# Kernel optimization log

Hardware: AMD Instinct MI355X
Metric: run time of the kernel (lower is better)

The kernel has to match this reference:

```python
import jax, jax.numpy as jnp
import numpy as np

NUM_OBS_OS = 8
NUM_OBS_TS = 6
HIDDEN = 128
NUM_ACTIONS = 9
B = 32768
N_TS = 32


def setup_inputs() -> dict:
    key = jax.random.key(0)
    ks = jax.random.split(key, 16)
    s_OS = jax.random.normal(ks[0], (B, NUM_OBS_OS), dtype=jnp.float32)
    s_TS = jax.random.normal(ks[1], (B, N_TS, NUM_OBS_TS), dtype=jnp.float32)
    # variable number of valid target ships per row (0..N_TS); trailing slots -> NaN
    lengths = jax.random.randint(ks[2], (B,), 0, N_TS + 1)
    pad = jnp.arange(N_TS)[None, :] >= lengths[:, None]          # [B, N_TS]
    s_TS = jnp.where(pad[:, :, None], jnp.nan, s_TS)
    s = jnp.concatenate([s_OS, s_TS.reshape(B, N_TS * NUM_OBS_TS)], axis=1)

    def lin(k, out_d, in_d):
        bound = 1.0 / np.sqrt(in_d)
        kw, kb = jax.random.split(k)
        W = jax.random.uniform(kw, (out_d, in_d), jnp.float32, -bound, bound)
        b = jax.random.uniform(kb, (out_d,), jnp.float32, -bound, bound)
        return W, b

    W_os, b_os = lin(ks[3], HIDDEN, NUM_OBS_OS)
    bound = 1.0 / np.sqrt(HIDDEN)
    W_ih = jax.random.uniform(ks[4], (4 * HIDDEN, NUM_OBS_TS), jnp.float32, -bound, bound)
    W_hh = jax.random.uniform(ks[5], (4 * HIDDEN, HIDDEN), jnp.float32, -bound, bound)
    b_ih = jax.random.uniform(ks[6], (4 * HIDDEN,), jnp.float32, -bound, bound)
    b_hh = jax.random.uniform(ks[7], (4 * HIDDEN,), jnp.float32, -bound, bound)
    W_ts, b_ts = lin(ks[8], HIDDEN, HIDDEN)
    W_c1, b_c1 = lin(ks[9], HIDDEN, 2 * HIDDEN)
    W_c2, b_c2 = lin(ks[10], NUM_ACTIONS, HIDDEN)
    return {"s": s, "W_os": W_os, "b_os": b_os, "W_ih": W_ih, "W_hh": W_hh,
            "b_ih": b_ih, "b_hh": b_hh, "W_ts": W_ts, "b_ts": b_ts,
            "W_c1": W_c1, "b_c1": b_c1, "W_c2": W_c2, "b_c2": b_c2}


def _lstm(x, W_ih, W_hh, b_ih, b_hh):
    """Single-layer batch-first LSTM; x: [B, T, I] -> outputs [B, T, H]."""
    Bc, T, _ = x.shape
    H = W_hh.shape[1]
    # precompute input projections for all steps: [T, B, 4H]
    xg = jnp.einsum('bti,gi->tbg', x, W_ih) + (b_ih + b_hh)

    def step(carry, xt):
        h, c = carry
        gates = xt + h @ W_hh.T                      # [B, 4H]
        i, f, g, o = jnp.split(gates, 4, axis=-1)    # torch order: i, f, g, o
        i = jax.nn.sigmoid(i)
        f = jax.nn.sigmoid(f)
        g = jnp.tanh(g)
        o = jax.nn.sigmoid(o)
        c = f * c + i * g
        h = o * jnp.tanh(c)
        return (h, c), h

    h0 = jnp.zeros((Bc, H), x.dtype)
    c0 = jnp.zeros((Bc, H), x.dtype)
    _, hs = jax.lax.scan(step, (h0, c0), xg)         # hs: [T, B, H]
    return jnp.transpose(hs, (1, 0, 2))


def reference(s, W_os, b_os, W_ih, W_hh, b_ih, b_hh, W_ts, b_ts, W_c1, b_c1, W_c2, b_c2):
    Bc = s.shape[0]
    s_OS = s[:, :NUM_OBS_OS]
    s_TS = s[:, NUM_OBS_OS:].reshape(Bc, -1, NUM_OBS_TS)          # [B, N_TS, 6]
    valid = jnp.logical_not(jnp.isnan(s_TS[:, :, 0]))             # [B, N_TS]
    n_obs = jnp.sum(valid, axis=1)                                # [B]
    h_idx = jnp.maximum(n_obs, 1) - 1                             # last valid step
    s_TS = jnp.where(jnp.isnan(s_TS), 0.0, s_TS)

    x_OS = jax.nn.relu(s_OS @ W_os.T + b_os)                      # [B, 128]

    out = _lstm(s_TS, W_ih, W_hh, b_ih, b_hh)                     # [B, N_TS, 128]
    x_TS = jnp.take_along_axis(out, h_idx[:, None, None], axis=1)[:, 0]  # [B, 128]
    x_TS = jnp.where((n_obs == 0)[:, None], 0.0, x_TS)
    x_TS = jax.nn.relu(x_TS @ W_ts.T + b_ts)

    x = jnp.concatenate([x_OS, x_TS], axis=1)                     # [B, 256]
    x = jax.nn.relu(x @ W_c1.T + b_c1)
    return x @ W_c2.T + b_c2                                      # [B, num_actions]
```

## Files before the change

kernel.cpp:

```cpp
#include <hip/hip_runtime.h>

#ifndef __has_builtin
#define __has_builtin(x) 0
#endif

#define NOBS_OS 8
#define NOBS_TS 6
#define HID 128
#define NACT 9
#define BTOT 32768
#define NTS 32
#define ROWS 16
#define NTILES 2048
#define QUADS 512
#define BLOCK 512
#define PREB 128

#define LEN_OFF 0
#define PERM_OFF BTOT
#define HIST_OFF (2 * BTOT)

typedef __attribute__((ext_vector_type(8))) short short8;
typedef __attribute__((ext_vector_type(4))) float f32x4;

__device__ inline unsigned short f2bf(float x) {
  unsigned int u = __float_as_uint(x);
  u += 0x7FFFu + ((u >> 16) & 1u);
  return (unsigned short)(u >> 16);
}

__device__ inline unsigned pkbf(float a, float b) {
#if __has_builtin(__builtin_amdgcn_cvt_pk_bf16_f32)
  auto v = __builtin_amdgcn_cvt_pk_bf16_f32(a, b);
  unsigned u;
  __builtin_memcpy(&u, &v, sizeof(u));
  return u;
#else
  return ((unsigned)f2bf(b) << 16) | (unsigned)f2bf(a);
#endif
}

__device__ inline float fexp2(float x) {
#if __has_builtin(__builtin_amdgcn_exp2f)
  return __builtin_amdgcn_exp2f(x);
#else
  return exp2f(x);
#endif
}
__device__ inline float frcp_(float x) {
#if __has_builtin(__builtin_amdgcn_rcpf)
  return __builtin_amdgcn_rcpf(x);
#else
  return 1.0f / x;
#endif
}

__device__ inline short8 pack8(f32x4 a, f32x4 b) {
  union { unsigned u[4]; short8 s; } r;
  r.u[0] = pkbf(a[0], a[1]); r.u[1] = pkbf(a[2], a[3]);
  r.u[2] = pkbf(b[0], b[1]); r.u[3] = pkbf(b[2], b[3]);
  return r.s;
}

__device__ inline short8 pack8s(const float* p, float s) {
  union { unsigned u[4]; short8 r; } r;
#pragma unroll
  for (int i = 0; i < 4; ++i) r.u[i] = pkbf(p[2 * i] * s, p[2 * i + 1] * s);
  return r.r;
}

__global__ void count_kernel(const float* __restrict__ s, int* __restrict__ ws) {
  __shared__ int lh[NTS + 1];
  const int tid = threadIdx.x;
  if (tid <= NTS) lh[tid] = 0;
  __syncthreads();
  const int row = blockIdx.x * 256 + tid;
  const float* p = s + (size_t)row * 200 + NOBS_OS;
  int lo = 0, hi = NTS;
  while (lo < hi) {
    const int mid = (lo + hi) >> 1;
    const float v = p[mid * NOBS_TS];
    if (v == v) lo = mid + 1; else hi = mid;
  }
  ws[LEN_OFF + row] = lo;
  atomicAdd(&lh[lo], 1);
  __syncthreads();
  if (tid <= NTS) ws[HIST_OFF + blockIdx.x * (NTS + 1) + tid] = lh[tid];
}

__global__ void scatter_kernel(int* __restrict__ ws) {
  __shared__ int tot[NTS + 1], pre[NTS + 1], gb[NTS + 1], lh[NTS + 1];
  const int tid = threadIdx.x;
  if (tid <= NTS) {
    int t = 0, pr = 0;
    for (int k = 0; k < PREB; ++k) {
      const int h = ws[HIST_OFF + k * (NTS + 1) + tid];
      t += h;
      if (k < (int)blockIdx.x) pr += h;
    }
    tot[tid] = t;
    pre[tid] = pr;
    lh[tid] = 0;
  }
  __syncthreads();
  if (tid == 0) {
    int a = 0;
    for (int b = 0; b <= NTS; ++b) { gb[b] = a; a += tot[b]; }
  }
  __syncthreads();
  const int row = blockIdx.x * 256 + tid;
  const int len = ws[LEN_OFF + row];
  const int r = atomicAdd(&lh[len], 1);
  __syncthreads();
  ws[PERM_OFF + gb[len] + pre[len] + r] = row;
}


#define GX(CN, T)                                                            \
  {                                                                          \
    short8 ax = z8;                                                          \
    if (q == 0) ax = *(const short8*)&x_st[CN][c * 264 + (T) * 8];           \
    _Pragma("unroll") for (int a = 0; a < 4; ++a)                            \
        acc[CN][a] = __builtin_amdgcn_mfma_f32_16x16x32_bf16(                \
            ax, Bh[a][4], biasv[a], 0, 0, 0);                                \
  }

#define GH(CN, T)                                                            \
  {                                                                          \
    const unsigned short* hb = hA[CN][((T) + 1) & 1];                        \
    _Pragma("unroll") for (int kt = 0; kt < 4; ++kt) {                       \
      const short8 ah = *(const short8*)&hb[kt * 512 + L * 8];               \
      _Pragma("unroll") for (int a = 0; a < 4; ++a)                          \
          acc[CN][a] = __builtin_amdgcn_mfma_f32_16x16x32_bf16(              \
              ah, Bh[a][kt], acc[CN][a], 0, 0, 0);                           \
    }                                                                        \
  }

#define ACT(CN, T)                                                           \
  {                                                                          \
    unsigned short* hw = &hA[CN][(T) & 1][pbase];                            \
    float hv[4];                                                             \
    _Pragma("unroll") for (int r = 0; r < 4; ++r) {                          \
      const float ei = fexp2(acc[CN][0][r]);                                 \
      const float ef = fexp2(acc[CN][1][r]);                                 \
      const float eg = fexp2(acc[CN][2][r]);                                 \
      const float eo = fexp2(acc[CN][3][r]);                                 \
      const float rig = frcp_((1.0f + ei) * (1.0f + eg));                    \
      const float rf = frcp_(1.0f + ef);                                     \
      const float cv = cc[CN][r] * rf + (1.0f - eg) * rig;                   \
      cc[CN][r] = cv;                                                        \
      const float ec = fexp2(cv * -2.88539008f);                             \
      const float roc = frcp_((1.0f + eo) * (1.0f + ec));                    \
      hv[r] = (1.0f - ec) * roc;                                             \
    }                                                                        \
    const unsigned p01 = pkbf(hv[0], hv[1]);                                 \
    const unsigned p23 = pkbf(hv[2], hv[3]);                                 \
    hw[0] = (unsigned short)p01;                                             \
    hw[8] = (unsigned short)(p01 >> 16);                                     \
    hw[16] = (unsigned short)p23;                                            \
    hw[24] = (unsigned short)(p23 >> 16);                                    \
    _Pragma("unroll") for (int r = 0; r < 4; ++r) {                          \
      if (((tpck[CN] >> (r * 8)) & 255u) == (unsigned)(T))                   \
        xts[CN][r] = hv[r];                                                  \
    }                                                                        \
  }

__global__ __launch_bounds__(BLOCK, 2) void recdqn_kernel(
    const float* __restrict__ s, const float* __restrict__ W_os,
    const float* __restrict__ b_os, const float* __restrict__ W_ih,
    const float* __restrict__ W_hh, const float* __restrict__ b_ih,
    const float* __restrict__ b_hh, const float* __restrict__ W_ts,
    const float* __restrict__ b_ts, const float* __restrict__ W_c1,
    const float* __restrict__ b_c1, const float* __restrict__ W_c2,
    const float* __restrict__ b_c2, const int* __restrict__ ws,
    float* __restrict__ out) {
  __shared__ unsigned short x_st[4][ROWS * 264];
  __shared__ unsigned short hA[4][2][2048];
  __shared__ unsigned short xtsb[4][2048];
  __shared__ unsigned short xcat[4096];
  __shared__ unsigned short x2b[2048];
  __shared__ int n_lds[4][ROWS];
  __shared__ int rid_s[4][ROWS];
  __shared__ int tmax_sh[4];

  const int tid = threadIdx.x;
  const int L = tid & 63;
  const int w = tid >> 6;
  const int c = L & 15;
  const int q = L >> 4;
  const int j = (w << 4) | c;

  const short8 z8 = {0, 0, 0, 0, 0, 0, 0, 0};

  short8 Bh[4][5];
  f32x4 biasv[4];
#pragma unroll
  for (int a = 0; a < 4; ++a) {
    const float sc = (a == 2) ? -2.88539008f : -1.44269504f;
    const int n = (a << 7) + j;
    const float bb = sc * (b_ih[n] + b_hh[n]);
    f32x4 bv = {bb, bb, bb, bb};
    biasv[a] = bv;
#pragma unroll
    for (int kt = 0; kt < 4; ++kt)
      Bh[a][kt] = pack8s(W_hh + n * HID + kt * 32 + q * 8, sc);
    short8 fx = z8;
    if (q == 0) {
      const float* px = W_ih + n * NOBS_TS;
      union { unsigned u[4]; short8 s; } fu;
      fu.u[0] = pkbf(px[0] * sc, px[1] * sc);
      fu.u[1] = pkbf(px[2] * sc, px[3] * sc);
      fu.u[2] = pkbf(px[4] * sc, px[5] * sc);
      fu.u[3] = 0;
      fx = fu.s;
    }
    Bh[a][4] = fx;
  }

  const int pbase = ((j >> 5) << 9) + (((j >> 3) & 3) << 7) + (q << 5) + (j & 7);

  const int p = (QUADS - 1) - blockIdx.x;
  if (tid < 64) {
    const int cn = tid >> 4, rr = tid & 15;
    const int row = ws[PERM_OFF + (4 * p + cn) * ROWS + rr];
    rid_s[cn][rr] = row;
    n_lds[cn][rr] = ws[LEN_OFF + row];
  }
  __syncthreads();

#pragma unroll
  for (int it = 0; it < 4; ++it) {
    const int slot = tid + it * 512;
    const int cn = slot >> 9, rt = slot & 511, r = rt >> 5, tq = rt & 31;
    short8 v = z8;
    if (tq < n_lds[cn][r]) {
      const float2* ps =
          (const float2*)(s + (size_t)rid_s[cn][r] * 200 + NOBS_OS + tq * NOBS_TS);
      const float2 A = ps[0], Bv = ps[1], Cv = ps[2];
      union { unsigned u[4]; short8 s; } vu;
      vu.u[0] = pkbf(A.x, A.y);
      vu.u[1] = pkbf(Bv.x, Bv.y);
      vu.u[2] = pkbf(Cv.x, Cv.y);
      vu.u[3] = 0;
      v = vu.s;
    }
    *(short8*)&x_st[cn][r * 264 + tq * 8] = v;
  }
  if (tid == 0) {
#pragma unroll
    for (int cn = 0; cn < 4; ++cn) {
      int mx = 0;
      for (int r = 0; r < ROWS; ++r) mx = max(mx, n_lds[cn][r]);
      tmax_sh[cn] = mx;
    }
  }
  __syncthreads();

  const int tm0 = tmax_sh[0], tm1 = tmax_sh[1];
  const int tm2 = tmax_sh[2], tm3 = tmax_sh[3];
  unsigned tpck[4];
#pragma unroll
  for (int cn = 0; cn < 4; ++cn) {
    unsigned pk = 0;
#pragma unroll
    for (int b = 0; b < 4; ++b)
      pk |= ((unsigned)((n_lds[cn][q * 4 + b] - 1) & 255)) << (b * 8);
    tpck[cn] = pk;
  }

  float cc[4][4], xts[4][4];
#pragma unroll
  for (int i = 0; i < 4; ++i) {
    cc[0][i] = 0.0f; cc[1][i] = 0.0f; cc[2][i] = 0.0f; cc[3][i] = 0.0f;
    xts[0][i] = 0.0f; xts[1][i] = 0.0f; xts[2][i] = 0.0f; xts[3][i] = 0.0f;
  }

  f32x4 acc[4][4];
  if (tm3 > 0) {
    if (tm0 > 0) GX(0, 0)
    if (tm1 > 0) GX(1, 0)
    if (tm2 > 0) GX(2, 0)
    GX(3, 0)
    if (tm0 > 0) ACT(0, 0)
    if (tm1 > 0) ACT(1, 0)
    if (tm2 > 0) ACT(2, 0)
    ACT(3, 0)
    __syncthreads();
    int t = 1;
    for (; t < tm0; ++t) {
      GX(0, t) GH(0, t)
      GX(1, t) GH(1, t)
      GX(2, t) GH(2, t)
      GX(3, t) GH(3, t)
      ACT(0, t) ACT(1, t) ACT(2, t) ACT(3, t)
      __syncthreads();
    }
    for (; t < tm1; ++t) {
      GX(1, t) GH(1, t)
      GX(2, t) GH(2, t)
      GX(3, t) GH(3, t)
      ACT(1, t) ACT(2, t) ACT(3, t)
      __syncthreads();
    }
    for (; t < tm2; ++t) {
      GX(2, t) GH(2, t)
      GX(3, t) GH(3, t)
      ACT(2, t) ACT(3, t)
      __syncthreads();
    }
    for (; t < tm3; ++t) {
      GX(3, t) GH(3, t)
      ACT(3, t)
      __syncthreads();
    }
  }

#pragma unroll
  for (int cn = 0; cn < 4; ++cn) {
    const unsigned p01 = pkbf(xts[cn][0], xts[cn][1]);
    const unsigned p23 = pkbf(xts[cn][2], xts[cn][3]);
    unsigned short* pw = &xtsb[cn][pbase];
    pw[0] = (unsigned short)p01;
    pw[8] = (unsigned short)(p01 >> 16);
    pw[16] = (unsigned short)p23;
    pw[24] = (unsigned short)(p23 >> 16);
  }
  __syncthreads();

  short8 Fts[4], Fc1[8], Fc2[4], bosf = z8;
#pragma unroll
  for (int kt = 0; kt < 4; ++kt) {
    const f32x4* pp = (const f32x4*)(W_ts + j * HID + kt * 32 + q * 8);
    Fts[kt] = pack8(pp[0], pp[1]);
  }
#pragma unroll
  for (int kt = 0; kt < 8; ++kt) {
    const f32x4* pp = (const f32x4*)(W_c1 + j * 256 + kt * 32 + q * 8);
    Fc1[kt] = pack8(pp[0], pp[1]);
  }
#pragma unroll
  for (int kt = 0; kt < 4; ++kt) Fc2[kt] = z8;
  if (w == 0 && c < NACT) {
#pragma unroll
    for (int kt = 0; kt < 4; ++kt) {
      const f32x4* pp = (const f32x4*)(W_c2 + c * HID + kt * 32 + q * 8);
      Fc2[kt] = pack8(pp[0], pp[1]);
    }
  }
  if (q == 0) {
    const f32x4* pb = (const f32x4*)(W_os + j * NOBS_OS);
    bosf = pack8(pb[0], pb[1]);
  }
  const float bts = b_ts[j], bc1 = b_c1[j], bos = b_os[j];
  const float bc2 = (w == 0 && c < NACT) ? b_c2[c] : 0.0f;

#pragma unroll 1
  for (int cn = 0; cn < 4; ++cn) {
    {
      f32x4 a2 = {bts, bts, bts, bts};
#pragma unroll
      for (int kt = 0; kt < 4; ++kt) {
        const short8 af = *(const short8*)&xtsb[cn][kt * 512 + L * 8];
        a2 = __builtin_amdgcn_mfma_f32_16x16x32_bf16(af, Fts[kt], a2, 0, 0, 0);
      }
      const unsigned p01 = pkbf(fmaxf(a2[0], 0.0f), fmaxf(a2[1], 0.0f));
      const unsigned p23 = pkbf(fmaxf(a2[2], 0.0f), fmaxf(a2[3], 0.0f));
      xcat[2048 + pbase + 0] = (unsigned short)p01;
      xcat[2048 + pbase + 8] = (unsigned short)(p01 >> 16);
      xcat[2048 + pbase + 16] = (unsigned short)p23;
      xcat[2048 + pbase + 24] = (unsigned short)(p23 >> 16);
    }
    {
      short8 aos = z8;
      if (q == 0) {
        const f32x4* pa = (const f32x4*)(s + (size_t)rid_s[cn][c] * 200);
        aos = pack8(pa[0], pa[1]);
      }
      f32x4 a2 = {bos, bos, bos, bos};
      a2 = __builtin_amdgcn_mfma_f32_16x16x32_bf16(aos, bosf, a2, 0, 0, 0);
      const unsigned p01 = pkbf(fmaxf(a2[0], 0.0f), fmaxf(a2[1], 0.0f));
      const unsigned p23 = pkbf(fmaxf(a2[2], 0.0f), fmaxf(a2[3], 0.0f));
      xcat[pbase + 0] = (unsigned short)p01;
      xcat[pbase + 8] = (unsigned short)(p01 >> 16);
      xcat[pbase + 16] = (unsigned short)p23;
      xcat[pbase + 24] = (unsigned short)(p23 >> 16);
    }
    __syncthreads();
    {
      f32x4 a2 = {bc1, bc1, bc1, bc1};
#pragma unroll
      for (int kt = 0; kt < 8; ++kt) {
        const short8 af = *(const short8*)&xcat[kt * 512 + L * 8];
        a2 = __builtin_amdgcn_mfma_f32_16x16x32_bf16(af, Fc1[kt], a2, 0, 0, 0);
      }
      const unsigned p01 = pkbf(fmaxf(a2[0], 0.0f), fmaxf(a2[1], 0.0f));
      const unsigned p23 = pkbf(fmaxf(a2[2], 0.0f), fmaxf(a2[3], 0.0f));
      x2b[pbase + 0] = (unsigned short)p01;
      x2b[pbase + 8] = (unsigned short)(p01 >> 16);
      x2b[pbase + 16] = (unsigned short)p23;
      x2b[pbase + 24] = (unsigned short)(p23 >> 16);
    }
    __syncthreads();
    if (w == 0) {
      f32x4 accf = {bc2, bc2, bc2, bc2};
#pragma unroll
      for (int kt = 0; kt < 4; ++kt) {
        const short8 af = *(const short8*)&x2b[kt * 512 + L * 8];
        accf = __builtin_amdgcn_mfma_f32_16x16x32_bf16(af, Fc2[kt], accf, 0, 0, 0);
      }
      if (c < NACT) {
#pragma unroll
        for (int r = 0; r < 4; ++r)
          out[(size_t)rid_s[cn][q * 4 + r] * NACT + c] = accf[r];
      }
    }
    __syncthreads();
  }
}

extern "C" void kernel_launch(void* const* d_in, const int* in_sizes, int n_in,
                              void* d_out, int out_size, void* d_ws, size_t ws_size,
                              hipStream_t stream) {
  (void)in_sizes; (void)n_in; (void)out_size; (void)ws_size;
  const float* s    = (const float*)d_in[0];
  const float* W_os = (const float*)d_in[1];
  const float* b_os = (const float*)d_in[2];
  const float* W_ih = (const float*)d_in[3];
  const float* W_hh = (const float*)d_in[4];
  const float* b_ih = (const float*)d_in[5];
  const float* b_hh = (const float*)d_in[6];
  const float* W_ts = (const float*)d_in[7];
  const float* b_ts = (const float*)d_in[8];
  const float* W_c1 = (const float*)d_in[9];
  const float* b_c1 = (const float*)d_in[10];
  const float* W_c2 = (const float*)d_in[11];
  const float* b_c2 = (const float*)d_in[12];
  int* ws = (int*)d_ws;
  float* outp = (float*)d_out;

  count_kernel<<<PREB, 256, 0, stream>>>(s, ws);
  scatter_kernel<<<PREB, 256, 0, stream>>>(ws);
  recdqn_kernel<<<QUADS, BLOCK, 0, stream>>>(
      s, W_os, b_os, W_ih, W_hh, b_ih, b_hh, W_ts, b_ts, W_c1, b_c1, W_c2,
      b_c2, ws, outp);
}
```

Measured before the change: 245.6 us.

## Process two 16-row tiles per block instead of four to double grid size

Each block now runs the LSTM recurrence for 2 tiles of 16 rows rather than 4, launching 1024 blocks instead of 512 and raising the launch-bounds occupancy hint from 2 to 4 blocks per CU. Shared memory and per-thread register state (cell and accumulator arrays) shrink by half, which lets more blocks co-reside and spreads the work over more waves. The cost is fewer independent MFMA chains interleaved per barrier step to hide latency, and the W_hh fragments are loaded into registers by twice as many blocks.

Measured after the change: 554.1 us. 2.26x slower.

```diff
diff --git a/kernel.cpp b/kernel.cpp
--- a/kernel.cpp
+++ b/kernel.cpp
@@ -12,7 +12,7 @@
 #define NTS 32
 #define ROWS 16
 #define NTILES 2048
-#define QUADS 512
+#define PAIRS 1024
 #define BLOCK 512
 #define PREB 128
 
@@ -165,7 +165,7 @@
     }                                                                        \
   }
 
-__global__ __launch_bounds__(BLOCK, 2) void recdqn_kernel(
+__global__ __launch_bounds__(BLOCK, 4) void recdqn_kernel(
     const float* __restrict__ s, const float* __restrict__ W_os,
     const float* __restrict__ b_os, const float* __restrict__ W_ih,
     const float* __restrict__ W_hh, const float* __restrict__ b_ih,
@@ -174,14 +174,14 @@
     const float* __restrict__ b_c1, const float* __restrict__ W_c2,
     const float* __restrict__ b_c2, const int* __restrict__ ws,
     float* __restrict__ out) {
-  __shared__ unsigned short x_st[4][ROWS * 264];
-  __shared__ unsigned short hA[4][2][2048];
-  __shared__ unsigned short xtsb[4][2048];
+  __shared__ unsigned short x_st[2][ROWS * 264];
+  __shared__ unsigned short hA[2][2][2048];
+  __shared__ unsigned short xtsb[2][2048];
   __shared__ unsigned short xcat[4096];
   __shared__ unsigned short x2b[2048];
-  __shared__ int n_lds[4][ROWS];
-  __shared__ int rid_s[4][ROWS];
-  __shared__ int tmax_sh[4];
+  __shared__ int n_lds[2][ROWS];
+  __shared__ int rid_s[2][ROWS];
+  __shared__ int tmax_sh[2];
 
   const int tid = threadIdx.x;
   const int L = tid & 63;
@@ -219,17 +219,17 @@
 
   const int pbase = ((j >> 5) << 9) + (((j >> 3) & 3) << 7) + (q << 5) + (j & 7);
 
-  const int p = (QUADS - 1) - blockIdx.x;
-  if (tid < 64) {
+  const int p = (PAIRS - 1) - blockIdx.x;
+  if (tid < 32) {
     const int cn = tid >> 4, rr = tid & 15;
-    const int row = ws[PERM_OFF + (4 * p + cn) * ROWS + rr];
+    const int row = ws[PERM_OFF + (2 * p + cn) * ROWS + rr];
     rid_s[cn][rr] = row;
     n_lds[cn][rr] = ws[LEN_OFF + row];
   }
   __syncthreads();
 
 #pragma unroll
-  for (int it = 0; it < 4; ++it) {
+  for (int it = 0; it < 2; ++it) {
     const int slot = tid + it * 512;
     const int cn = slot >> 9, rt = slot & 511, r = rt >> 5, tq = rt & 31;
     short8 v = z8;
@@ -248,7 +248,7 @@
   }
   if (tid == 0) {
 #pragma unroll
-    for (int cn = 0; cn < 4; ++cn) {
+    for (int cn = 0; cn < 2; ++cn) {
       int mx = 0;
       for (int r = 0; r < ROWS; ++r) mx = max(mx, n_lds[cn][r]);
       tmax_sh[cn] = mx;
@@ -257,10 +257,9 @@
   __syncthreads();
 
   const int tm0 = tmax_sh[0], tm1 = tmax_sh[1];
-  const int tm2 = tmax_sh[2], tm3 = tmax_sh[3];
-  unsigned tpck[4];
-#pragma unroll
-  for (int cn = 0; cn < 4; ++cn) {
+  unsigned tpck[2];
+#pragma unroll
+  for (int cn = 0; cn < 2; ++cn) {
     unsigned pk = 0;
 #pragma unroll
     for (int b = 0; b < 4; ++b)
@@ -268,55 +267,36 @@
     tpck[cn] = pk;
   }
 
-  float cc[4][4], xts[4][4];
+  float cc[2][4], xts[2][4];
 #pragma unroll
   for (int i = 0; i < 4; ++i) {
-    cc[0][i] = 0.0f; cc[1][i] = 0.0f; cc[2][i] = 0.0f; cc[3][i] = 0.0f;
-    xts[0][i] = 0.0f; xts[1][i] = 0.0f; xts[2][i] = 0.0f; xts[3][i] = 0.0f;
-  }
-
-  f32x4 acc[4][4];
-  if (tm3 > 0) {
+    cc[0][i] = 0.0f; cc[1][i] = 0.0f;
+    xts[0][i] = 0.0f; xts[1][i] = 0.0f;
+  }
+
+  f32x4 acc[2][4];
+  if (tm1 > 0) {
     if (tm0 > 0) GX(0, 0)
-    if (tm1 > 0) GX(1, 0)
-    if (tm2 > 0) GX(2, 0)
-    GX(3, 0)
+    GX(1, 0)
     if (tm0 > 0) ACT(0, 0)
-    if (tm1 > 0) ACT(1, 0)
-    if (tm2 > 0) ACT(2, 0)
-    ACT(3, 0)
+    ACT(1, 0)
     __syncthreads();
     int t = 1;
     for (; t < tm0; ++t) {
       GX(0, t) GH(0, t)
       GX(1, t) GH(1, t)
-      GX(2, t) GH(2, t)
-      GX(3, t) GH(3, t)
-      ACT(0, t) ACT(1, t) ACT(2, t) ACT(3, t)
+      ACT(0, t) ACT(1, t)
       __syncthreads();
     }
     for (; t < tm1; ++t) {
       GX(1, t) GH(1, t)
-      GX(2, t) GH(2, t)
-      GX(3, t) GH(3, t)
-      ACT(1, t) ACT(2, t) ACT(3, t)
+      ACT(1, t)
       __syncthreads();
     }
-    for (; t < tm2; ++t) {
-      GX(2, t) GH(2, t)
-      GX(3, t) GH(3, t)
-      ACT(2, t) ACT(3, t)
-      __syncthreads();
-    }
-    for (; t < tm3; ++t) {
-      GX(3, t) GH(3, t)
-      ACT(3, t)
-      __syncthreads();
-    }
-  }
-
-#pragma unroll
-  for (int cn = 0; cn < 4; ++cn) {
+  }
+
+#pragma unroll
+  for (int cn = 0; cn < 2; ++cn) {
     const unsigned p01 = pkbf(xts[cn][0], xts[cn][1]);
     const unsigned p23 = pkbf(xts[cn][2], xts[cn][3]);
     unsigned short* pw = &xtsb[cn][pbase];
@@ -355,7 +335,7 @@
   const float bc2 = (w == 0 && c < NACT) ? b_c2[c] : 0.0f;
 
 #pragma unroll 1
-  for (int cn = 0; cn < 4; ++cn) {
+  for (int cn = 0; cn < 2; ++cn) {
     {
       f32x4 a2 = {bts, bts, bts, bts};
 #pragma unroll
@@ -440,7 +420,7 @@
 
   count_kernel<<<PREB, 256, 0, stream>>>(s, ws);
   scatter_kernel<<<PREB, 256, 0, stream>>>(ws);
-  recdqn_kernel<<<QUADS, BLOCK, 0, stream>>>(
+  recdqn_kernel<<<PAIRS, BLOCK, 0, stream>>>(
       s, W_os, b_os, W_ih, W_hh, b_ih, b_hh, W_ts, b_ts, W_c1, b_c1, W_c2,
       b_c2, ws, outp);
 }
```

## Prefetch next-step input gates, batch head across chunks, merge LSTM reciprocals

Applied to the files above, without the earlier changes.

The LSTM loop now computes the input-projection MFMAs (GX) for step t+1 after the activations of step t and before the barrier, so the input-gate work sits in the slack around the h-dependent GH and ACT phases. The post-LSTM head is restructured to process all four row chunks in each stage, with two barriers in total instead of three per chunk. Its intermediate buffers are aliased onto the now-dead hA and xtsb LDS arrays to free shared memory. The cell update also folds two reciprocals into one by cross-multiplying, which trades a transcendental for extra multiplies and may lose some float range.

Result: slower. 251.2 us (+2.3%).

```diff
diff --git a/kernel.cpp b/kernel.cpp
--- a/kernel.cpp
+++ b/kernel.cpp
@@ -145,9 +145,10 @@
       const float ef = fexp2(acc[CN][1][r]);                                 \
       const float eg = fexp2(acc[CN][2][r]);                                 \
       const float eo = fexp2(acc[CN][3][r]);                                 \
-      const float rig = frcp_((1.0f + ei) * (1.0f + eg));                    \
-      const float rf = frcp_(1.0f + ef);                                     \
-      const float cv = cc[CN][r] * rf + (1.0f - eg) * rig;                   \
+      const float P = (1.0f + ei) * (1.0f + eg);                             \
+      const float fp = 1.0f + ef;                                            \
+      const float num = cc[CN][r] * P + (1.0f - eg) * fp;                    \
+      const float cv = num * frcp_(fp * P);                                  \
       cc[CN][r] = cv;                                                        \
       const float ec = fexp2(cv * -2.88539008f);                             \
       const float roc = frcp_((1.0f + eo) * (1.0f + ec));                    \
@@ -177,11 +178,11 @@
   __shared__ unsigned short x_st[4][ROWS * 264];
   __shared__ unsigned short hA[4][2][2048];
   __shared__ unsigned short xtsb[4][2048];
-  __shared__ unsigned short xcat[4096];
-  __shared__ unsigned short x2b[2048];
   __shared__ int n_lds[4][ROWS];
   __shared__ int rid_s[4][ROWS];
   __shared__ int tmax_sh[4];
+  unsigned short* xcat_al = &hA[0][0][0];
+  unsigned short* x2b_al = &xtsb[0][0];
 
   const int tid = threadIdx.x;
   const int L = tid & 63;
@@ -285,32 +286,34 @@
     if (tm1 > 0) ACT(1, 0)
     if (tm2 > 0) ACT(2, 0)
     ACT(3, 0)
+    if (tm0 > 1) GX(0, 1)
+    if (tm1 > 1) GX(1, 1)
+    if (tm2 > 1) GX(2, 1)
+    if (tm3 > 1) GX(3, 1)
     __syncthreads();
     int t = 1;
     for (; t < tm0; ++t) {
-      GX(0, t) GH(0, t)
-      GX(1, t) GH(1, t)
-      GX(2, t) GH(2, t)
-      GX(3, t) GH(3, t)
+      GH(0, t) GH(1, t) GH(2, t) GH(3, t)
       ACT(0, t) ACT(1, t) ACT(2, t) ACT(3, t)
+      GX(0, t + 1) GX(1, t + 1) GX(2, t + 1) GX(3, t + 1)
       __syncthreads();
     }
     for (; t < tm1; ++t) {
-      GX(1, t) GH(1, t)
-      GX(2, t) GH(2, t)
-      GX(3, t) GH(3, t)
+      GH(1, t) GH(2, t) GH(3, t)
       ACT(1, t) ACT(2, t) ACT(3, t)
+      GX(1, t + 1) GX(2, t + 1) GX(3, t + 1)
       __syncthreads();
     }
     for (; t < tm2; ++t) {
-      GX(2, t) GH(2, t)
-      GX(3, t) GH(3, t)
+      GH(2, t) GH(3, t)
       ACT(2, t) ACT(3, t)
+      GX(2, t + 1) GX(3, t + 1)
       __syncthreads();
     }
     for (; t < tm3; ++t) {
-      GX(3, t) GH(3, t)
+      GH(3, t)
       ACT(3, t)
+      GX(3, t + 1)
       __syncthreads();
     }
   }
@@ -354,58 +357,66 @@
   const float bts = b_ts[j], bc1 = b_c1[j], bos = b_os[j];
   const float bc2 = (w == 0 && c < NACT) ? b_c2[c] : 0.0f;
 
-#pragma unroll 1
+#pragma unroll
   for (int cn = 0; cn < 4; ++cn) {
-    {
-      f32x4 a2 = {bts, bts, bts, bts};
+    f32x4 a2 = {bts, bts, bts, bts};
+#pragma unroll
+    for (int kt = 0; kt < 4; ++kt) {
+      const short8 af = *(const short8*)&xtsb[cn][kt * 512 + L * 8];
+      a2 = __builtin_amdgcn_mfma_f32_16x16x32_bf16(af, Fts[kt], a2, 0, 0, 0);
+    }
+    const unsigned p01 = pkbf(fmaxf(a2[0], 0.0f), fmaxf(a2[1], 0.0f));
+    const unsigned p23 = pkbf(fmaxf(a2[2], 0.0f), fmaxf(a2[3], 0.0f));
+    unsigned short* xc = xcat_al + cn * 4096 + 2048 + pbase;
+    xc[0] = (unsigned short)p01;
+    xc[8] = (unsigned short)(p01 >> 16);
+    xc[16] = (unsigned short)p23;
+    xc[24] = (unsigned short)(p23 >> 16);
+  }
+#pragma unroll
+  for (int cn = 0; cn < 4; ++cn) {
+    short8 aos = z8;
+    if (q == 0) {
+      const f32x4* pa = (const f32x4*)(s + (size_t)rid_s[cn][c] * 200);
+      aos = pack8(pa[0], pa[1]);
+    }
+    f32x4 a2 = {bos, bos, bos, bos};
+    a2 = __builtin_amdgcn_mfma_f32_16x16x32_bf16(aos, bosf, a2, 0, 0, 0);
+    const unsigned p01 = pkbf(fmaxf(a2[0], 0.0f), fmaxf(a2[1], 0.0f));
+    const unsigned p23 = pkbf(fmaxf(a2[2], 0.0f), fmaxf(a2[3], 0.0f));
+    unsigned short* xc = xcat_al + cn * 4096 + pbase;
+    xc[0] = (unsigned short)p01;
+    xc[8] = (unsigned short)(p01 >> 16);
+    xc[16] = (unsigned short)p23;
+    xc[24] = (unsigned short)(p23 >> 16);
+  }
+  __syncthreads();
+
+#pragma unroll
+  for (int cn = 0; cn < 4; ++cn) {
+    f32x4 a2 = {bc1, bc1, bc1, bc1};
+#pragma unroll
+    for (int kt = 0; kt < 8; ++kt) {
+      const short8 af = *(const short8*)&xcat_al[cn * 4096 + kt * 512 + L * 8];
+      a2 = __builtin_amdgcn_mfma_f32_16x16x32_bf16(af, Fc1[kt], a2, 0, 0, 0);
+    }
+    const unsigned p01 = pkbf(fmaxf(a2[0], 0.0f), fmaxf(a2[1], 0.0f));
+    const unsigned p23 = pkbf(fmaxf(a2[2], 0.0f), fmaxf(a2[3], 0.0f));
+    unsigned short* xb = x2b_al + cn * 2048 + pbase;
+    xb[0] = (unsigned short)p01;
+    xb[8] = (unsigned short)(p01 >> 16);
+    xb[16] = (unsigned short)p23;
+    xb[24] = (unsigned short)(p23 >> 16);
+  }
+  __syncthreads();
+
+  if (w == 0) {
+#pragma unroll
+    for (int cn = 0; cn < 4; ++cn) {
+      f32x4 accf = {bc2, bc2, bc2, bc2};
 #pragma unroll
       for (int kt = 0; kt < 4; ++kt) {
-        const short8 af = *(const short8*)&xtsb[cn][kt * 512 + L * 8];
-        a2 = __builtin_amdgcn_mfma_f32_16x16x32_bf16(af, Fts[kt], a2, 0, 0, 0);
-      }
-      const unsigned p01 = pkbf(fmaxf(a2[0], 0.0f), fmaxf(a2[1], 0.0f));
-      const unsigned p23 = pkbf(fmaxf(a2[2], 0.0f), fmaxf(a2[3], 0.0f));
-      xcat[2048 + pbase + 0] = (unsigned short)p01;
-      xcat[2048 + pbase + 8] = (unsigned short)(p01 >> 16);
-      xcat[2048 + pbase + 16] = (unsigned short)p23;
-      xcat[2048 + pbase + 24] = (unsigned short)(p23 >> 16);
-    }
-    {
-      short8 aos = z8;
-      if (q == 0) {
-        const f32x4* pa = (const f32x4*)(s + (size_t)rid_s[cn][c] * 200);
-        aos = pack8(pa[0], pa[1]);
-      }
-      f32x4 a2 = {bos, bos, bos, bos};
-      a2 = __builtin_amdgcn_mfma_f32_16x16x32_bf16(aos, bosf, a2, 0, 0, 0);
-      const unsigned p01 = pkbf(fmaxf(a2[0], 0.0f), fmaxf(a2[1], 0.0f));
-      const unsigned p23 = pkbf(fmaxf(a2[2], 0.0f), fmaxf(a2[3], 0.0f));
-      xcat[pbase + 0] = (unsigned short)p01;
-      xcat[pbase + 8] = (unsigned short)(p01 >> 16);
-      xcat[pbase + 16] = (unsigned short)p23;
-      xcat[pbase + 24] = (unsigned short)(p23 >> 16);
-    }
-    __syncthreads();
-    {
-      f32x4 a2 = {bc1, bc1, bc1, bc1};
-#pragma unroll
-      for (int kt = 0; kt < 8; ++kt) {
-        const short8 af = *(const short8*)&xcat[kt * 512 + L * 8];
-        a2 = __builtin_amdgcn_mfma_f32_16x16x32_bf16(af, Fc1[kt], a2, 0, 0, 0);
-      }
-      const unsigned p01 = pkbf(fmaxf(a2[0], 0.0f), fmaxf(a2[1], 0.0f));
-      const unsigned p23 = pkbf(fmaxf(a2[2], 0.0f), fmaxf(a2[3], 0.0f));
-      x2b[pbase + 0] = (unsigned short)p01;
-      x2b[pbase + 8] = (unsigned short)(p01 >> 16);
-      x2b[pbase + 16] = (unsigned short)p23;
-      x2b[pbase + 24] = (unsigned short)(p23 >> 16);
-    }
-    __syncthreads();
-    if (w == 0) {
-      f32x4 accf = {bc2, bc2, bc2, bc2};
-#pragma unroll
-      for (int kt = 0; kt < 4; ++kt) {
-        const short8 af = *(const short8*)&x2b[kt * 512 + L * 8];
+        const short8 af = *(const short8*)&x2b_al[cn * 2048 + kt * 512 + L * 8];
         accf = __builtin_amdgcn_mfma_f32_16x16x32_bf16(af, Fc2[kt], accf, 0, 0, 0);
       }
       if (c < NACT) {
@@ -414,7 +425,6 @@
           out[(size_t)rid_s[cn][q * 4 + r] * NACT + c] = accf[r];
       }
     }
-    __syncthreads();
   }
 }
 
```
